# Performance work log

Hardware: AMD Instinct MI355X
Metric: run time of the kernel (lower is better)

The kernel has to match this reference:

```python
import jax, jax.numpy as jnp
import numpy as np

N = 150000
E = 600000
IN_DIM = 128
HID = 64


def setup_inputs() -> dict:
    key = jax.random.key(0)
    ks = jax.random.split(key, 8)
    obs = jax.random.normal(ks[0], (N, IN_DIM), dtype=jnp.float32)
    edge_index = jax.random.randint(ks[1], (2, E), 0, N, dtype=jnp.int64)
    # GCNConv / Linear parameters (PyTorch layout: W is [out, in])
    W1 = jax.random.normal(ks[2], (HID, IN_DIM), dtype=jnp.float32) / np.sqrt(IN_DIM)
    b1 = jnp.zeros((HID,), dtype=jnp.float32)
    W2 = jax.random.normal(ks[3], (HID, HID), dtype=jnp.float32) / np.sqrt(HID)
    b2 = jnp.zeros((HID,), dtype=jnp.float32)
    W3 = jax.random.normal(ks[4], (1, HID), dtype=jnp.float32) / np.sqrt(HID)
    b3 = jnp.zeros((1,), dtype=jnp.float32)
    return {"obs": obs, "edge_index": edge_index, "W1": W1, "b1": b1,
            "W2": W2, "b2": b2, "W3": W3, "b3": b3}


def _gcn_norm(edge_index, n):
    # PyG gcn_norm: add self-loops, symmetric normalization D^-1/2 A D^-1/2
    loops = jnp.arange(n, dtype=edge_index.dtype)
    row = jnp.concatenate([edge_index[0], loops])  # source
    col = jnp.concatenate([edge_index[1], loops])  # target
    deg = jax.ops.segment_sum(jnp.ones(row.shape[0], jnp.float32), col, num_segments=n)
    dinv = jnp.where(deg > 0, jax.lax.rsqrt(deg), 0.0)
    norm = dinv[row] * dinv[col]  # [E+N]
    return row, col, norm


def _gcn_conv(x, row, col, norm, n, W, b):
    # x' = lin(x); out[col] += norm * x'[row]; out += bias
    xw = x @ W.T                     # [N, out]
    msg = xw[row] * norm[:, None]    # gather + scale, [E+N, out]
    out = jax.ops.segment_sum(msg, col, num_segments=n)
    return out + b


def reference(obs, edge_index, W1, b1, W2, b2, W3, b3):
    n = obs.shape[0]
    row, col, norm = _gcn_norm(edge_index, n)
    h1 = jax.nn.relu(_gcn_conv(obs, row, col, norm, n, W1, b1))
    h2 = jax.nn.relu(_gcn_conv(h1, row, col, norm, n, W2, b2))
    out = h2 @ W3.T + b3             # [N, 1]
    out = out.reshape(-1, 15)[:, 3:].reshape(-1)  # drop first 3 of every 15
    return out
```

## Files before the change

kernel.cpp:

```cpp
#include <hip/hip_runtime.h>

#define NN 150000
#define NE 600000
#define IND 128
#define HID 64
#define KMAX 32
#define BSHIFT 8
#define NBUCK 586
#define SUBCAP 224
#define PARTB 586
#define GEMM_GRID ((NN + 63) / 64)
#define NOUT 120000

typedef short s16x8 __attribute__((ext_vector_type(8)));
typedef float f32x4 __attribute__((ext_vector_type(4)));

__device__ __forceinline__ unsigned f2bf(float f) {
    unsigned u = __float_as_uint(f);
    return (u + 0x7FFFu + ((u >> 16) & 1u)) >> 16;
}

#define ACC4(v, dr) \
    a0 = fmaf(__uint_as_float((v).x << 16), dr, a0); \
    a1 = fmaf(__uint_as_float((v).x & 0xFFFF0000u), dr, a1); \
    a2 = fmaf(__uint_as_float((v).y << 16), dr, a2); \
    a3 = fmaf(__uint_as_float((v).y & 0xFFFF0000u), dr, a3);

__global__ void k_zero(int* __restrict__ gcnt) {
    int t = blockIdx.x * 256 + threadIdx.x;
    if (t < NBUCK * 8) gcnt[t] = 0;
}

__global__ __launch_bounds__(256) void k_init(
        const int* __restrict__ rowv, const int* __restrict__ colv,
        int* __restrict__ gcnt, int2* __restrict__ ebuf,
        const float* __restrict__ obs, const float* __restrict__ W1,
        unsigned short* __restrict__ xs) {
    __shared__ char smem[64 * IND * 2];
    int tid = threadIdx.x;
    if (blockIdx.x < PARTB) {
        int* hist  = (int*)smem;
        int* bases = hist + NBUCK;
        for (int i = tid; i < NBUCK; i += 256) hist[i] = 0;
        __syncthreads();
        int t = blockIdx.x * 256 + tid;
        bool valid = (t < NE / 4);
        int4 r4, c4;
        int bk[4], sl[4];
        if (valid) {
            r4 = ((const int4*)rowv)[t];
            c4 = ((const int4*)colv)[t];
            bk[0] = c4.x >> BSHIFT; sl[0] = atomicAdd(&hist[bk[0]], 1);
            bk[1] = c4.y >> BSHIFT; sl[1] = atomicAdd(&hist[bk[1]], 1);
            bk[2] = c4.z >> BSHIFT; sl[2] = atomicAdd(&hist[bk[2]], 1);
            bk[3] = c4.w >> BSHIFT; sl[3] = atomicAdd(&hist[bk[3]], 1);
        }
        __syncthreads();
        int xcd = blockIdx.x & 7;
        for (int i = tid; i < NBUCK; i += 256)
            bases[i] = hist[i] ? atomicAdd(&gcnt[i * 8 + xcd], hist[i]) : 0;
        __syncthreads();
        if (valid) {
            #pragma unroll
            for (int e = 0; e < 4; ++e) {
                int c = (e == 0) ? c4.x : (e == 1) ? c4.y : (e == 2) ? c4.z : c4.w;
                int r = (e == 0) ? r4.x : (e == 1) ? r4.y : (e == 2) ? r4.z : r4.w;
                int p = bases[bk[e]] + sl[e];
                if (p < SUBCAP) ebuf[(bk[e] * 8 + xcd) * SUBCAP + p] = make_int2(c, r);
            }
        }
        return;
    }
    char* sB = smem;
    int base = (blockIdx.x - PARTB) * 64;

    {
        const float4* Wsrc = (const float4*)W1;
        for (int idx = tid; idx < 64 * 32; idx += 256) {
            int row = idx >> 5, c4i = idx & 31;
            float4 w = Wsrc[idx];
            uint2 p;
            p.x = f2bf(w.x) | (f2bf(w.y) << 16);
            p.y = f2bf(w.z) | (f2bf(w.w) << 16);
            int byte = row * (IND * 2) + c4i * 8;
            byte ^= (row & 7) << 4;
            *(uint2*)(sB + byte) = p;
        }
    }
    __syncthreads();

    int wave = tid >> 6, lane = tid & 63;
    int r16 = lane & 15, kg = lane >> 4;
    int arow = base + 16 * wave + r16;
    if (arow >= NN) arow = NN - 1;
    const float4* Ap = (const float4*)(obs + (size_t)arow * IND) + kg * 2;

    float4 va[8];
    #pragma unroll
    for (int s = 0; s < 4; ++s) {
        va[2 * s]     = Ap[s * 8];
        va[2 * s + 1] = Ap[s * 8 + 1];
    }

    f32x4 acc[4];
    #pragma unroll
    for (int j = 0; j < 4; ++j) acc[j] = (f32x4){0.f, 0.f, 0.f, 0.f};

    #pragma unroll
    for (int s = 0; s < 4; ++s) {
        float4 v0 = va[2 * s], v1 = va[2 * s + 1];
        s16x8 a;
        a[0] = (short)f2bf(v0.x); a[1] = (short)f2bf(v0.y);
        a[2] = (short)f2bf(v0.z); a[3] = (short)f2bf(v0.w);
        a[4] = (short)f2bf(v1.x); a[5] = (short)f2bf(v1.y);
        a[6] = (short)f2bf(v1.z); a[7] = (short)f2bf(v1.w);
        int kb = (s * 32 + kg * 8) * 2;
        #pragma unroll
        for (int j = 0; j < 4; ++j) {
            int row = 16 * j + r16;
            int byte = row * (IND * 2) + kb;
            byte ^= (row & 7) << 4;
            s16x8 b = *(const s16x8*)(sB + byte);
            acc[j] = __builtin_amdgcn_mfma_f32_16x16x32_bf16(a, b, acc[j], 0, 0, 0);
        }
    }

    #pragma unroll
    for (int r = 0; r < 4; ++r) {
        int n = base + 16 * wave + kg * 4 + r;
        if (n >= NN) continue;
        #pragma unroll
        for (int j = 0; j < 4; ++j) {
            int c = 16 * j + r16;
            xs[(size_t)n * HID + c] = (unsigned short)f2bf(acc[j][r]);
        }
    }
}

__global__ __launch_bounds__(256) void k_sort(
        const int* __restrict__ gcnt, const int2* __restrict__ ebuf,
        int* __restrict__ cursor, float* __restrict__ dinvf,
        int* __restrict__ csr_src) {
    __shared__ int cnt[256];
    int tid = threadIdx.x;
    int k = blockIdx.x;
    int lo = k << BSHIFT;
    cnt[tid] = 0;
    __syncthreads();
    for (int x = 0; x < 8; ++x) {
        int len = gcnt[k * 8 + x]; if (len > SUBCAP) len = SUBCAP;
        const int2* run = ebuf + (size_t)(k * 8 + x) * SUBCAP;
        for (int i = tid; i < len; i += 256) {
            int2 e = run[i];
            int s = atomicAdd(&cnt[e.x - lo], 1);
            if (s < KMAX) csr_src[e.x * KMAX + s] = e.y;
        }
    }
    __syncthreads();
    int n = lo + tid;
    if (n < NN) {
        cursor[n] = cnt[tid];
        dinvf[n] = rsqrtf((float)(cnt[tid] + 1));
    }
}

__global__ __launch_bounds__(256) void k_agg_gemm(
        const unsigned short* __restrict__ xs, const int* __restrict__ cursor,
        const float* __restrict__ dinvf, const int* __restrict__ csr_src,
        const float* __restrict__ bias, const float* __restrict__ W2,
        unsigned short* __restrict__ xs2) {
    __shared__ char smem[2 * 64 * HID * 2];
    char* sA = smem;
    char* sB = smem + 64 * HID * 2;
    int tid = threadIdx.x;
    int base = blockIdx.x * 64;

    {
        const float4* Wsrc = (const float4*)W2;
        for (int idx = tid; idx < 64 * 16; idx += 256) {
            int row = idx >> 4, c4i = idx & 15;
            float4 w = Wsrc[idx];
            uint2 p;
            p.x = f2bf(w.x) | (f2bf(w.y) << 16);
            p.y = f2bf(w.z) | (f2bf(w.w) << 16);
            int byte = row * (HID * 2) + c4i * 8;
            byte ^= (row & 7) << 4;
            *(uint2*)(sB + byte) = p;
        }
    }

    int lane = tid & 63;
    int l16 = lane & 15, gbase = lane & 48;
    int grp = tid >> 4;
    const uint2* src = (const uint2*)xs;
    float4 bb = ((const float4*)bias)[l16];

    int degA[4], cntA[4], idxA[4];
    uint2 svA[4];
    float drA[4];
    #pragma unroll
    for (int s4 = 0; s4 < 4; ++s4) {
        int node = base + s4 * 16 + grp;
        bool ok = node < NN;
        int nc = ok ? node : NN - 1;
        int deg = cursor[nc];
        degA[s4] = deg;
        cntA[s4] = ok ? (deg < KMAX ? deg : KMAX) : 0;
        idxA[s4] = csr_src[nc * KMAX + l16];
        svA[s4]  = src[(size_t)nc * 16 + l16];
    }
    #pragma unroll
    for (int s4 = 0; s4 < 4; ++s4) {
        drA[s4] = (l16 < cntA[s4]) ? dinvf[idxA[s4]] : 0.0f;
    }

    #pragma unroll
    for (int s4 = 0; s4 < 4; ++s4) {
        int row = s4 * 16 + grp;
        int node = base + row;
        int cnt = cntA[s4];
        float dn = rsqrtf((float)(degA[s4] + 1));
        uint2 sv = svA[s4];
        float a0 = __uint_as_float(sv.x << 16) * dn;
        float a1 = __uint_as_float(sv.x & 0xFFFF0000u) * dn;
        float a2 = __uint_as_float(sv.y << 16) * dn;
        float a3 = __uint_as_float(sv.y & 0xFFFF0000u) * dn;
        uint2 v[8];
        #pragma unroll
        for (int j = 0; j < 8; ++j) {
            int r = __shfl(idxA[s4], gbase + j, 64);
            r = (j < cnt) ? r : 0;
            v[j] = src[(size_t)r * 16 + l16];
        }
        #pragma unroll
        for (int j = 0; j < 8; ++j) {
            float dr = __shfl(drA[s4], gbase + j, 64);
            ACC4(v[j], dr)
        }
        if (cnt > 8) {
            int c16 = cnt < 16 ? cnt : 16;
            for (int j = 8; j < c16; ++j) {
                int r    = __shfl(idxA[s4], gbase + j, 64);
                float dr = __shfl(drA[s4], gbase + j, 64);
                uint2 vv = src[(size_t)r * 16 + l16];
                ACC4(vv, dr)
            }
            for (int j = 16; j < cnt; ++j) {
                int r = csr_src[node * KMAX + j];
                float dr = dinvf[r];
                uint2 vv = src[(size_t)r * 16 + l16];
                ACC4(vv, dr)
            }
        }
        float h0 = fmaxf(fmaf(dn, a0, bb.x), 0.f);
        float h1 = fmaxf(fmaf(dn, a1, bb.y), 0.f);
        float h2 = fmaxf(fmaf(dn, a2, bb.z), 0.f);
        float h3 = fmaxf(fmaf(dn, a3, bb.w), 0.f);
        uint2 o;
        o.x = f2bf(h0) | (f2bf(h1) << 16);
        o.y = f2bf(h2) | (f2bf(h3) << 16);
        if (node >= NN) { o.x = 0u; o.y = 0u; }
        int byte = row * (HID * 2) + l16 * 8;
        byte ^= (row & 7) << 4;
        *(uint2*)(sA + byte) = o;
    }
    __syncthreads();

    int wave = tid >> 6;
    int wr = wave >> 1, wc = wave & 1;
    int r16 = lane & 15, kg = lane >> 4;

    f32x4 acc[2][2];
    #pragma unroll
    for (int i = 0; i < 2; ++i)
        #pragma unroll
        for (int j = 0; j < 2; ++j)
            acc[i][j] = (f32x4){0.f, 0.f, 0.f, 0.f};

    #pragma unroll
    for (int s = 0; s < HID / 32; ++s) {
        int kb = (s * 32 + kg * 8) * 2;
        s16x8 a[2], b[2];
        #pragma unroll
        for (int i = 0; i < 2; ++i) {
            int row = 32 * wr + 16 * i + r16;
            int byte = row * (HID * 2) + kb;
            byte ^= (row & 7) << 4;
            a[i] = *(const s16x8*)(sA + byte);
        }
        #pragma unroll
        for (int j = 0; j < 2; ++j) {
            int row = 32 * wc + 16 * j + r16;
            int byte = row * (HID * 2) + kb;
            byte ^= (row & 7) << 4;
            b[j] = *(const s16x8*)(sB + byte);
        }
        #pragma unroll
        for (int i = 0; i < 2; ++i)
            #pragma unroll
            for (int j = 0; j < 2; ++j)
                acc[i][j] = __builtin_amdgcn_mfma_f32_16x16x32_bf16(a[i], b[j], acc[i][j], 0, 0, 0);
    }

    #pragma unroll
    for (int i = 0; i < 2; ++i) {
        #pragma unroll
        for (int r = 0; r < 4; ++r) {
            int n = base + 32 * wr + 16 * i + kg * 4 + r;
            if (n >= NN) continue;
            float d = dinvf[n];
            #pragma unroll
            for (int j = 0; j < 2; ++j) {
                int c = 32 * wc + 16 * j + r16;
                xs2[(size_t)n * HID + c] = (unsigned short)f2bf(acc[i][j][r] * d);
            }
        }
    }
}

__global__ __launch_bounds__(256) void k_agg_out(const unsigned short* __restrict__ xs,
                      const int* __restrict__ cursor, const int* __restrict__ csr_src,
                      const float* __restrict__ bias, const float* __restrict__ W3,
                      const float* __restrict__ b3, float* __restrict__ outp) {
    int tid = threadIdx.x;
    int lane = tid & 63;
    int l16 = lane & 15, gbase = lane & 48;
    int q = blockIdx.x * 16 + (tid >> 4);
    if (q >= NOUT) return;
    int g15 = q / 12, jj12 = q - g15 * 12;
    int node = g15 * 15 + 3 + jj12;
    int deg = cursor[node];
    int cnt = deg < KMAX ? deg : KMAX;
    float dn = rsqrtf((float)(deg + 1));
    const uint2* src = (const uint2*)xs;
    int idx0 = csr_src[node * KMAX + l16];
    float w0 = (l16 < cnt) ? 1.0f : 0.0f;
    uint2 sv = src[(size_t)node * 16 + l16];
    float a0 = __uint_as_float(sv.x << 16);
    float a1 = __uint_as_float(sv.x & 0xFFFF0000u);
    float a2 = __uint_as_float(sv.y << 16);
    float a3 = __uint_as_float(sv.y & 0xFFFF0000u);
    uint2 v[8];
    #pragma unroll
    for (int j = 0; j < 8; ++j) {
        int r = __shfl(idx0, gbase + j, 64);
        r = (j < cnt) ? r : 0;
        v[j] = src[(size_t)r * 16 + l16];
    }
    #pragma unroll
    for (int j = 0; j < 8; ++j) {
        float w = __shfl(w0, gbase + j, 64);
        ACC4(v[j], w)
    }
    if (cnt > 8) {
        int c16 = cnt < 16 ? cnt : 16;
        for (int j = 8; j < c16; ++j) {
            int r = __shfl(idx0, gbase + j, 64);
            uint2 vv = src[(size_t)r * 16 + l16];
            ACC4(vv, 1.0f)
        }
        for (int j = 16; j < cnt; ++j) {
            int r = csr_src[node * KMAX + j];
            uint2 vv = src[(size_t)r * 16 + l16];
            ACC4(vv, 1.0f)
        }
    }
    float4 bb = ((const float4*)bias)[l16];
    float h0 = fmaxf(fmaf(dn, a0, bb.x), 0.f);
    float h1 = fmaxf(fmaf(dn, a1, bb.y), 0.f);
    float h2 = fmaxf(fmaf(dn, a2, bb.z), 0.f);
    float h3 = fmaxf(fmaf(dn, a3, bb.w), 0.f);
    float4 ww = ((const float4*)W3)[l16];
    float v3 = h0 * ww.x + h1 * ww.y + h2 * ww.z + h3 * ww.w;
    v3 += __shfl_xor(v3, 1, 64);
    v3 += __shfl_xor(v3, 2, 64);
    v3 += __shfl_xor(v3, 4, 64);
    v3 += __shfl_xor(v3, 8, 64);
    if (l16 == 0) outp[q] = v3 + b3[0];
}

extern "C" void kernel_launch(void* const* d_in, const int* in_sizes, int n_in,
                              void* d_out, int out_size, void* d_ws, size_t ws_size,
                              hipStream_t stream) {
    const float* obs = (const float*)d_in[0];
    const int*   ei  = (const int*)d_in[1];
    const float* W1  = (const float*)d_in[2];
    const float* b1  = (const float*)d_in[3];
    const float* W2  = (const float*)d_in[4];
    const float* b2  = (const float*)d_in[5];
    const float* W3  = (const float*)d_in[6];
    const float* b3  = (const float*)d_in[7];
    float* out = (float*)d_out;

    char* ws = (char*)d_ws;
    size_t off = 0;
    auto alloc = [&](size_t bytes) -> void* {
        void* p = ws + off;
        off += (bytes + 255) & ~(size_t)255;
        return p;
    };
    int*   gcnt    = (int*)  alloc((size_t)NBUCK * 8 * 4);
    int*   cursor  = (int*)  alloc((size_t)NN * 4);
    float* dinvf   = (float*)alloc((size_t)NN * 4);
    int*   csr_src = (int*)  alloc((size_t)NN * KMAX * 4);
    int2*  ebuf    = (int2*) alloc((size_t)NBUCK * 8 * SUBCAP * 8);
    unsigned short* XB  = (unsigned short*)alloc((size_t)NN * HID * 2);
    unsigned short* XB2 = (unsigned short*)alloc((size_t)NN * HID * 2);

    const int* rowv = ei;
    const int* colv = ei + NE;

    k_zero<<<(NBUCK * 8 + 255) / 256, 256, 0, stream>>>(gcnt);
    k_init<<<PARTB + GEMM_GRID, 256, 0, stream>>>(rowv, colv, gcnt, ebuf, obs, W1, XB);
    k_sort<<<NBUCK, 256, 0, stream>>>(gcnt, ebuf, cursor, dinvf, csr_src);
    k_agg_gemm<<<GEMM_GRID, 256, 0, stream>>>(XB, cursor, dinvf, csr_src, b1, W2, XB2);
    k_agg_out<<<(NOUT + 15) / 16, 256, 0, stream>>>(XB2, cursor, csr_src, b2, W3, b3, out);
}
```

Baseline: 107.8 us.

## Move GEMM1 to run alongside bucket sort instead of partition

Splits the edge partitioning into its own kernel, with each block now handling 512 int4 edge groups so half as many blocks run, and merges the per-bucket sort into the first GEMM kernel as extra blocks. The first-layer GEMM now overlaps with the sort stage rather than the partition stage, which rebalances the work across the two launches. Having fewer partition blocks cuts the number of global atomics on the bucket counters, but each block carries more registers and does less parallel work.

```diff
diff --git a/kernel.cpp b/kernel.cpp
--- a/kernel.cpp
+++ b/kernel.cpp
@@ -8,7 +8,7 @@
 #define BSHIFT 8
 #define NBUCK 586
 #define SUBCAP 224
-#define PARTB 586
+#define PARTB 293
 #define GEMM_GRID ((NN + 63) / 64)
 #define NOUT 120000
 
@@ -31,48 +31,82 @@
     if (t < NBUCK * 8) gcnt[t] = 0;
 }
 
-__global__ __launch_bounds__(256) void k_init(
+__global__ __launch_bounds__(256) void k_part(
         const int* __restrict__ rowv, const int* __restrict__ colv,
-        int* __restrict__ gcnt, int2* __restrict__ ebuf,
+        int* __restrict__ gcnt, int2* __restrict__ ebuf) {
+    __shared__ int hist[NBUCK];
+    __shared__ int bases[NBUCK];
+    int tid = threadIdx.x;
+    for (int i = tid; i < NBUCK; i += 256) hist[i] = 0;
+    __syncthreads();
+    int4 r4[2], c4[2];
+    int bk[8], sl[8];
+    bool val[2];
+    #pragma unroll
+    for (int h = 0; h < 2; ++h) {
+        int t = blockIdx.x * 512 + h * 256 + tid;
+        val[h] = (t < NE / 4);
+        if (val[h]) {
+            r4[h] = ((const int4*)rowv)[t];
+            c4[h] = ((const int4*)colv)[t];
+            bk[4*h+0] = c4[h].x >> BSHIFT; sl[4*h+0] = atomicAdd(&hist[bk[4*h+0]], 1);
+            bk[4*h+1] = c4[h].y >> BSHIFT; sl[4*h+1] = atomicAdd(&hist[bk[4*h+1]], 1);
+            bk[4*h+2] = c4[h].z >> BSHIFT; sl[4*h+2] = atomicAdd(&hist[bk[4*h+2]], 1);
+            bk[4*h+3] = c4[h].w >> BSHIFT; sl[4*h+3] = atomicAdd(&hist[bk[4*h+3]], 1);
+        }
+    }
+    __syncthreads();
+    int xcd = blockIdx.x & 7;
+    for (int i = tid; i < NBUCK; i += 256)
+        bases[i] = hist[i] ? atomicAdd(&gcnt[i * 8 + xcd], hist[i]) : 0;
+    __syncthreads();
+    #pragma unroll
+    for (int h = 0; h < 2; ++h) {
+        if (val[h]) {
+            #pragma unroll
+            for (int e = 0; e < 4; ++e) {
+                int c = (e == 0) ? c4[h].x : (e == 1) ? c4[h].y : (e == 2) ? c4[h].z : c4[h].w;
+                int r = (e == 0) ? r4[h].x : (e == 1) ? r4[h].y : (e == 2) ? r4[h].z : r4[h].w;
+                int p = bases[bk[4*h+e]] + sl[4*h+e];
+                if (p < SUBCAP) ebuf[(bk[4*h+e] * 8 + xcd) * SUBCAP + p] = make_int2(c, r);
+            }
+        }
+    }
+}
+
+__global__ __launch_bounds__(256) void k_sort_gemm1(
         const float* __restrict__ obs, const float* __restrict__ W1,
-        unsigned short* __restrict__ xs) {
+        unsigned short* __restrict__ xs,
+        const int* __restrict__ gcnt, const int2* __restrict__ ebuf,
+        int* __restrict__ cursor, float* __restrict__ dinvf,
+        int* __restrict__ csr_src) {
     __shared__ char smem[64 * IND * 2];
     int tid = threadIdx.x;
-    if (blockIdx.x < PARTB) {
-        int* hist  = (int*)smem;
-        int* bases = hist + NBUCK;
-        for (int i = tid; i < NBUCK; i += 256) hist[i] = 0;
+    if (blockIdx.x < NBUCK) {
+        int k = blockIdx.x;
+        int lo = k << BSHIFT;
+        int* cnt = (int*)smem;
+        cnt[tid] = 0;
         __syncthreads();
-        int t = blockIdx.x * 256 + tid;
-        bool valid = (t < NE / 4);
-        int4 r4, c4;
-        int bk[4], sl[4];
-        if (valid) {
-            r4 = ((const int4*)rowv)[t];
-            c4 = ((const int4*)colv)[t];
-            bk[0] = c4.x >> BSHIFT; sl[0] = atomicAdd(&hist[bk[0]], 1);
-            bk[1] = c4.y >> BSHIFT; sl[1] = atomicAdd(&hist[bk[1]], 1);
-            bk[2] = c4.z >> BSHIFT; sl[2] = atomicAdd(&hist[bk[2]], 1);
-            bk[3] = c4.w >> BSHIFT; sl[3] = atomicAdd(&hist[bk[3]], 1);
+        for (int x = 0; x < 8; ++x) {
+            int len = gcnt[k * 8 + x]; if (len > SUBCAP) len = SUBCAP;
+            const int2* run = ebuf + (size_t)(k * 8 + x) * SUBCAP;
+            for (int i = tid; i < len; i += 256) {
+                int2 e = run[i];
+                int s = atomicAdd(&cnt[e.x - lo], 1);
+                if (s < KMAX) csr_src[e.x * KMAX + s] = e.y;
+            }
         }
         __syncthreads();
-        int xcd = blockIdx.x & 7;
-        for (int i = tid; i < NBUCK; i += 256)
-            bases[i] = hist[i] ? atomicAdd(&gcnt[i * 8 + xcd], hist[i]) : 0;
-        __syncthreads();
-        if (valid) {
-            #pragma unroll
-            for (int e = 0; e < 4; ++e) {
-                int c = (e == 0) ? c4.x : (e == 1) ? c4.y : (e == 2) ? c4.z : c4.w;
-                int r = (e == 0) ? r4.x : (e == 1) ? r4.y : (e == 2) ? r4.z : r4.w;
-                int p = bases[bk[e]] + sl[e];
-                if (p < SUBCAP) ebuf[(bk[e] * 8 + xcd) * SUBCAP + p] = make_int2(c, r);
-            }
+        int n = lo + tid;
+        if (n < NN) {
+            cursor[n] = cnt[tid];
+            dinvf[n] = rsqrtf((float)(cnt[tid] + 1));
         }
         return;
     }
     char* sB = smem;
-    int base = (blockIdx.x - PARTB) * 64;
+    int base = (blockIdx.x - NBUCK) * 64;
 
     {
         const float4* Wsrc = (const float4*)W1;
@@ -134,33 +168,6 @@
             int c = 16 * j + r16;
             xs[(size_t)n * HID + c] = (unsigned short)f2bf(acc[j][r]);
         }
-    }
-}
-
-__global__ __launch_bounds__(256) void k_sort(
-        const int* __restrict__ gcnt, const int2* __restrict__ ebuf,
-        int* __restrict__ cursor, float* __restrict__ dinvf,
-        int* __restrict__ csr_src) {
-    __shared__ int cnt[256];
-    int tid = threadIdx.x;
-    int k = blockIdx.x;
-    int lo = k << BSHIFT;
-    cnt[tid] = 0;
-    __syncthreads();
-    for (int x = 0; x < 8; ++x) {
-        int len = gcnt[k * 8 + x]; if (len > SUBCAP) len = SUBCAP;
-        const int2* run = ebuf + (size_t)(k * 8 + x) * SUBCAP;
-        for (int i = tid; i < len; i += 256) {
-            int2 e = run[i];
-            int s = atomicAdd(&cnt[e.x - lo], 1);
-            if (s < KMAX) csr_src[e.x * KMAX + s] = e.y;
-        }
-    }
-    __syncthreads();
-    int n = lo + tid;
-    if (n < NN) {
-        cursor[n] = cnt[tid];
-        dinvf[n] = rsqrtf((float)(cnt[tid] + 1));
     }
 }
 
@@ -411,8 +418,9 @@
     const int* colv = ei + NE;
 
     k_zero<<<(NBUCK * 8 + 255) / 256, 256, 0, stream>>>(gcnt);
-    k_init<<<PARTB + GEMM_GRID, 256, 0, stream>>>(rowv, colv, gcnt, ebuf, obs, W1, XB);
-    k_sort<<<NBUCK, 256, 0, stream>>>(gcnt, ebuf, cursor, dinvf, csr_src);
+    k_part<<<PARTB, 256, 0, stream>>>(rowv, colv, gcnt, ebuf);
+    k_sort_gemm1<<<NBUCK + GEMM_GRID, 256, 0, stream>>>(obs, W1, XB, gcnt, ebuf,
+                                                        cursor, dinvf, csr_src);
     k_agg_gemm<<<GEMM_GRID, 256, 0, stream>>>(XB, cursor, dinvf, csr_src, b1, W2, XB2);
     k_agg_out<<<(NOUT + 15) / 16, 256, 0, stream>>>(XB2, cursor, csr_src, b2, W3, b3, out);
 }
```

New measurement: 95.53 us. 1.13x faster.
